# Optimization experiments

Measured on AMD Instinct MI355X. Metric: run time of the kernel, lower is better.

## Reference

```python
import jax, jax.numpy as jnp
import numpy as np

B, T = 32, 48
INPUT_DIM = 40000
TRAJ = 10
H = 256
OUT = 40000
TD = 48
L = 2
E = 128
DIN = E + TD  # 176


def setup_inputs() -> dict:
    key = jax.random.key(0)
    ks = jax.random.split(key, 16)
    s = 0.05
    inp = {
        "locations": jax.random.randint(ks[0], (B, T), 0, INPUT_DIM),
        "times": jax.random.randint(ks[1], (B, T), 0, TD),
        "labels": jax.random.randint(ks[2], (B,), 0, TRAJ),
        "embed_table": jax.random.normal(ks[3], (INPUT_DIM, E), dtype=jnp.float32) * s,
        "traj_table": jax.random.normal(ks[4], (TRAJ, H * L), dtype=jnp.float32) * s,
        "fc_w": jax.random.normal(ks[5], (OUT + TD, H), dtype=jnp.float32) * s,
        "fc_b": jnp.zeros((OUT + TD,), dtype=jnp.float32),
        "w_ih0": jax.random.normal(ks[6], (3 * H, DIN), dtype=jnp.float32) * s,
        "w_hh0": jax.random.normal(ks[7], (3 * H, H), dtype=jnp.float32) * s,
        "b_ih0": jnp.zeros((3 * H,), dtype=jnp.float32),
        "b_hh0": jnp.zeros((3 * H,), dtype=jnp.float32),
        "w_ih1": jax.random.normal(ks[8], (3 * H, H), dtype=jnp.float32) * s,
        "w_hh1": jax.random.normal(ks[9], (3 * H, H), dtype=jnp.float32) * s,
        "b_ih1": jnp.zeros((3 * H,), dtype=jnp.float32),
        "b_hh1": jnp.zeros((3 * H,), dtype=jnp.float32),
    }
    return inp


def gru_layer(x, h0, w_ih, w_hh, b_ih, b_hh):
    """PyTorch-semantics GRU layer. x: [T,B,din], h0: [B,H] -> [T,B,H]."""
    # precompute input projections for all timesteps (gates ordered r,z,n)
    xp = jnp.einsum('tbd,gd->tbg', x, w_ih) + b_ih  # [T,B,3H]

    def step(h, xp_t):
        hp = h @ w_hh.T + b_hh                      # [B,3H]
        xr, xz, xn = jnp.split(xp_t, 3, axis=-1)
        hr, hz, hn = jnp.split(hp, 3, axis=-1)
        r = jax.nn.sigmoid(xr + hr)
        z = jax.nn.sigmoid(xz + hz)
        n = jnp.tanh(xn + r * hn)
        h_new = (1.0 - z) * n + z * h
        return h_new, h_new

    _, ys = jax.lax.scan(step, h0, xp)
    return ys


def reference(locations, times, labels, embed_table, traj_table, fc_w, fc_b,
              w_ih0, w_hh0, b_ih0, b_hh0, w_ih1, w_hh1, b_ih1, b_hh1):
    x = embed_table[locations]                                  # [B,T,E]
    th = jax.nn.one_hot(times, TD, dtype=x.dtype)               # [B,T,TD]
    x = jnp.concatenate([x, th], axis=-1).transpose(1, 0, 2)    # [T,B,E+TD]
    # init_hidden: view (B, L*H) -> (L, -1, H), a raw reshape as in torch
    h0 = traj_table[labels].reshape(L, -1, H)                   # [L,B,H]
    y = gru_layer(x, h0[0], w_ih0, w_hh0, b_ih0, b_hh0)
    y = gru_layer(y, h0[1], w_ih1, w_hh1, b_ih1, b_hh1)         # [T,B,H]
    out = jax.nn.relu(y).transpose(1, 0, 2) @ fc_w.T + fc_b     # [B,T,OUT+TD]
    loc = jax.nn.log_softmax(out[..., :OUT], axis=-1)
    tm = jax.nn.log_softmax(out[..., OUT:], axis=-1)
    return loc, tm
```

## Files before the change

kernel.cpp:

```cpp
#include <hip/hip_runtime.h>
#include <math.h>

typedef __attribute__((ext_vector_type(4))) float f32x4;
typedef __attribute__((ext_vector_type(8))) short s16x8;

constexpr int B = 32, T = 48, H = 256, E = 128, TD = 48;
constexpr int OUT = 40000, NOUTC = 40048, NPADC = 40064;
constexpr int G3 = 768, DIN = 176;

__device__ __forceinline__ float sigmoidf_(float x){ return 1.f/(1.f+__expf(-x)); }
__device__ __forceinline__ float tanhf_(float x){
  float e = __expf(2.f*x);
  return 1.f - 2.f/(e + 1.f);
}
__device__ __forceinline__ unsigned short f2bf(float f){
  unsigned int u = __float_as_uint(f);
  u += 0x7fffu + ((u>>16)&1u);
  return (unsigned short)(u>>16);
}
__device__ __forceinline__ s16x8 pack8(float4 u, float4 v){
  s16x8 r;
  r[0]=(short)f2bf(u.x); r[1]=(short)f2bf(u.y); r[2]=(short)f2bf(u.z); r[3]=(short)f2bf(u.w);
  r[4]=(short)f2bf(v.x); r[5]=(short)f2bf(v.y); r[6]=(short)f2bf(v.z); r[7]=(short)f2bf(v.w);
  return r;
}
__device__ __forceinline__ void gl_lds16(const unsigned short* g, unsigned short* l){
  __builtin_amdgcn_global_load_lds((const __attribute__((address_space(1))) void*)g,
                                   (__attribute__((address_space(3))) void*)l, 16, 0, 0);
}
__device__ __forceinline__ void st_sc(unsigned* p, unsigned v){
  __hip_atomic_store(p, v, __ATOMIC_RELAXED, __HIP_MEMORY_SCOPE_SYSTEM);
}
__device__ __forceinline__ unsigned long long ld_sc64(const unsigned long long* p){
  return __hip_atomic_load(p, __ATOMIC_RELAXED, __HIP_MEMORY_SCOPE_SYSTEM);
}

__global__ void wt_kernel(const float* __restrict__ w_ih0, float* __restrict__ wT,
                          unsigned* __restrict__ bar){
  int i = blockIdx.x*256 + threadIdx.x;
  if (blockIdx.x == 0 && threadIdx.x == 0)
    __hip_atomic_store(bar, 0u, __ATOMIC_RELAXED, __HIP_MEMORY_SCOPE_SYSTEM);
  if (i >= E*G3) return;
  int e = i / G3, g = i % G3;
  wT[i] = w_ih0[g*DIN + e];
}

__global__ void xp0_kernel(const int* __restrict__ locations, const int* __restrict__ times,
                           const float* __restrict__ embed, const float* __restrict__ wT,
                           const float* __restrict__ w_ih0, const float* __restrict__ b_ih0,
                           float* __restrict__ xp0)
{
  __shared__ float emb_s[16][E];
  __shared__ int tm_s[16];
  const int r0 = blockIdx.x * 16;
  const int tid = threadIdx.x;
  for (int i = tid; i < 16*E; i += 256) {
    int p = i >> 7, e = i & 127;
    int r = r0 + p; int t = r >> 5, b = r & 31;
    emb_s[p][e] = embed[(size_t)locations[b*T + t]*E + e];
  }
  if (tid < 16) {
    int r = r0 + tid; int t = r >> 5, b = r & 31;
    tm_s[tid] = times[b*T + t];
  }
  __syncthreads();
  const int g = tid;
  float acc[16][3];
  #pragma unroll
  for (int p=0;p<16;p++){acc[p][0]=0.f;acc[p][1]=0.f;acc[p][2]=0.f;}
  for (int e = 0; e < E; e += 4) {
    float w0_[4], w1_[4], w2_[4];
    #pragma unroll
    for (int i=0;i<4;i++){
      w0_[i]=wT[(e+i)*G3 + g];
      w1_[i]=wT[(e+i)*G3 + 256 + g];
      w2_[i]=wT[(e+i)*G3 + 512 + g];
    }
    #pragma unroll
    for (int p=0;p<16;p++){
      float4 ev = *(const float4*)&emb_s[p][e];
      acc[p][0] += ev.x*w0_[0]+ev.y*w0_[1]+ev.z*w0_[2]+ev.w*w0_[3];
      acc[p][1] += ev.x*w1_[0]+ev.y*w1_[1]+ev.z*w1_[2]+ev.w*w1_[3];
      acc[p][2] += ev.x*w2_[0]+ev.y*w2_[1]+ev.z*w2_[2]+ev.w*w2_[3];
    }
  }
  #pragma unroll
  for (int p=0;p<16;p++){
    int r = r0+p; int tt = tm_s[p];
    xp0[(size_t)r*G3 + g]       = acc[p][0] + b_ih0[g]     + w_ih0[g*DIN       + E + tt];
    xp0[(size_t)r*G3 + 256 + g] = acc[p][1] + b_ih0[g+256] + w_ih0[(g+256)*DIN + E + tt];
    xp0[(size_t)r*G3 + 512 + g] = acc[p][2] + b_ih0[g+512] + w_ih0[(g+512)*DIN + E + tt];
  }
}

struct GruArgs {
  const float* xp0; const float* traj; const int* labels;
  const float* w_hh0; const float* b_hh0;
  const float* w_ih1; const float* w_hh1; const float* b_ih1; const float* b_hh1;
  unsigned short* exch;
  unsigned* bar;
  unsigned short* abf;
};

__global__ void __launch_bounds__(384, 2) gru_kernel(GruArgs a)
{
  __shared__ unsigned short Ash[2][32*264];
  __shared__ float gl0[3*32*17];
  __shared__ float gl1[4*32*17];
  __shared__ float hF0[512];
  __shared__ float hF1[512];
  const int tid  = threadIdx.x;
  const int jt   = blockIdx.x;
  const int wv   = tid >> 6;
  const int lane = tid & 63;
  const int g    = wv % 3, mt = wv / 3;
  const int fn   = lane & 15;
  const int fq   = lane >> 4;
  unsigned* exch32 = (unsigned*)a.exch;

  const int row = g*256 + jt*16 + fn;
  s16x8 b0[8], b1[16];
  #pragma unroll
  for (int kk = 0; kk < 8; ++kk) {
    const float* p0 = a.w_hh0 + (size_t)row*H + kk*32 + fq*8;
    const float* p1 = a.w_ih1 + (size_t)row*H + kk*32 + fq*8;
    const float* p2 = a.w_hh1 + (size_t)row*H + kk*32 + fq*8;
    b0[kk]    = pack8(*(const float4*)p0, *(const float4*)(p0+4));
    b1[kk]    = pack8(*(const float4*)p1, *(const float4*)(p1+4));
    b1[kk+8]  = pack8(*(const float4*)p2, *(const float4*)(p2+4));
  }

  for (int i = tid; i < 2*B*H; i += 384) {
    int l = i >> 13, bb = (i >> 8) & 31, h = i & 255;
    float v = a.traj[(size_t)a.labels[l*16 + (bb>>1)]*512 + (bb&1)*256 + h];
    Ash[l][bb*264 + h] = f2bf(v);
  }
  if (tid < 256) {
    int b = tid >> 3, jp = tid & 7, j0 = jp*2, gj = jt*16 + j0;
    float v00 = a.traj[(size_t)a.labels[(b>>1)]*512      + (b&1)*256 + gj];
    float v01 = a.traj[(size_t)a.labels[(b>>1)]*512      + (b&1)*256 + gj+1];
    float v10 = a.traj[(size_t)a.labels[16 + (b>>1)]*512 + (b&1)*256 + gj];
    float v11 = a.traj[(size_t)a.labels[16 + (b>>1)]*512 + (b&1)*256 + gj+1];
    hF0[b*16+j0] = v00; hF0[b*16+j0+1] = v01;
    hF1[b*16+j0] = v10; hF1[b*16+j0+1] = v11;
    st_sc(&exch32[(1*2+1)*4096 + b*128 + jt*8 + jp],
          (unsigned)f2bf(v10) | ((unsigned)f2bf(v11) << 16));
  }

  for (int p = 0; p <= T; ++p) {
    const int cur = p & 1, nxt = cur ^ 1;
    if (p) {
      const unsigned long long* src = (const unsigned long long*)a.exch + (size_t)cur*4096;
      unsigned long long v[11];
      #pragma unroll
      for (int k = 0; k < 11; ++k) {
        int i = tid + k*384;
        if (i < 4096) v[k] = ld_sc64(&src[i]);
      }
      #pragma unroll
      for (int k = 0; k < 11; ++k) {
        int i = tid + k*384;
        if (i < 4096) {
          int st = i >> 11, bb = (i >> 6) & 31, k4 = (i & 63) << 2;
          *(unsigned long long*)&Ash[st][bb*264 + k4] = v[k];
        }
      }
    }
    __syncthreads();

    if (p < T) {
      f32x4 acc = (f32x4){0.f,0.f,0.f,0.f};
      #pragma unroll
      for (int kk = 0; kk < 8; ++kk) {
        s16x8 af = *(const s16x8*)&Ash[0][(mt*16 + fn)*264 + kk*32 + fq*8];
        acc = __builtin_amdgcn_mfma_f32_16x16x32_bf16(af, b0[kk], acc, 0, 0, 0);
      }
      #pragma unroll
      for (int i = 0; i < 4; ++i)
        gl0[(g*32 + mt*16 + fq*4 + i)*17 + fn] = acc[i];
    }
    if (p >= 1) {
      if (g < 2) {
        f32x4 acc = (f32x4){0.f,0.f,0.f,0.f};
        #pragma unroll
        for (int kk = 0; kk < 8; ++kk) {
          s16x8 af = *(const s16x8*)&Ash[0][(mt*16 + fn)*264 + kk*32 + fq*8];
          acc = __builtin_amdgcn_mfma_f32_16x16x32_bf16(af, b1[kk], acc, 0, 0, 0);
        }
        #pragma unroll
        for (int kk = 0; kk < 8; ++kk) {
          s16x8 af = *(const s16x8*)&Ash[1][(mt*16 + fn)*264 + kk*32 + fq*8];
          acc = __builtin_amdgcn_mfma_f32_16x16x32_bf16(af, b1[8+kk], acc, 0, 0, 0);
        }
        #pragma unroll
        for (int i = 0; i < 4; ++i)
          gl1[(g*32 + mt*16 + fq*4 + i)*17 + fn] = acc[i];
      } else {
        f32x4 ax = (f32x4){0.f,0.f,0.f,0.f}, ah = (f32x4){0.f,0.f,0.f,0.f};
        #pragma unroll
        for (int kk = 0; kk < 8; ++kk) {
          s16x8 afx = *(const s16x8*)&Ash[0][(mt*16 + fn)*264 + kk*32 + fq*8];
          s16x8 afh = *(const s16x8*)&Ash[1][(mt*16 + fn)*264 + kk*32 + fq*8];
          ax = __builtin_amdgcn_mfma_f32_16x16x32_bf16(afx, b1[kk],   ax, 0, 0, 0);
          ah = __builtin_amdgcn_mfma_f32_16x16x32_bf16(afh, b1[8+kk], ah, 0, 0, 0);
        }
        #pragma unroll
        for (int i = 0; i < 4; ++i) {
          gl1[(2*32 + mt*16 + fq*4 + i)*17 + fn] = ax[i];
          gl1[(3*32 + mt*16 + fq*4 + i)*17 + fn] = ah[i];
        }
      }
    }
    __syncthreads();

    if (tid < 256) {
      const int b = tid >> 3, jp = tid & 7, j0 = jp*2, gj = jt*16 + j0;
      if (p < T) {
        const float* xp = a.xp0 + (size_t)(p*B + b)*G3 + gj;
        float r0 = sigmoidf_(xp[0]   + gl0[(b)*17+j0]      + a.b_hh0[gj]);
        float r1 = sigmoidf_(xp[1]   + gl0[(b)*17+j0+1]    + a.b_hh0[gj+1]);
        float z0 = sigmoidf_(xp[256] + gl0[(32+b)*17+j0]   + a.b_hh0[256+gj]);
        float z1 = sigmoidf_(xp[257] + gl0[(32+b)*17+j0+1] + a.b_hh0[256+gj+1]);
        float n0 = tanhf_(xp[512] + r0*(gl0[(64+b)*17+j0]   + a.b_hh0[512+gj]));
        float n1 = tanhf_(xp[513] + r1*(gl0[(64+b)*17+j0+1] + a.b_hh0[512+gj+1]));
        float h0n = (1.f - z0)*n0 + z0*hF0[b*16+j0];
        float h1n = (1.f - z1)*n1 + z1*hF0[b*16+j0+1];
        hF0[b*16+j0] = h0n; hF0[b*16+j0+1] = h1n;
        st_sc(&exch32[(nxt*2 + 0)*4096 + b*128 + jt*8 + jp],
              (unsigned)f2bf(h0n) | ((unsigned)f2bf(h1n) << 16));
      }
      if (p >= 1) {
        const int t1 = p - 1;
        float r0 = sigmoidf_(gl1[(b)*17+j0]      + a.b_ih1[gj]     + a.b_hh1[gj]);
        float r1 = sigmoidf_(gl1[(b)*17+j0+1]    + a.b_ih1[gj+1]   + a.b_hh1[gj+1]);
        float z0 = sigmoidf_(gl1[(32+b)*17+j0]   + a.b_ih1[256+gj]   + a.b_hh1[256+gj]);
        float z1 = sigmoidf_(gl1[(32+b)*17+j0+1] + a.b_ih1[256+gj+1] + a.b_hh1[256+gj+1]);
        float n0 = tanhf_(gl1[(64+b)*17+j0]   + a.b_ih1[512+gj]
                          + r0*(gl1[(96+b)*17+j0]   + a.b_hh1[512+gj]));
        float n1 = tanhf_(gl1[(64+b)*17+j0+1] + a.b_ih1[512+gj+1]
                          + r1*(gl1[(96+b)*17+j0+1] + a.b_hh1[512+gj+1]));
        float h0n = (1.f - z0)*n0 + z0*hF1[b*16+j0];
        float h1n = (1.f - z1)*n1 + z1*hF1[b*16+j0+1];
        hF1[b*16+j0] = h0n; hF1[b*16+j0+1] = h1n;
        st_sc(&exch32[(nxt*2 + 1)*4096 + b*128 + jt*8 + jp],
              (unsigned)f2bf(h0n) | ((unsigned)f2bf(h1n) << 16));
        ((unsigned*)a.abf)[((size_t)(b*T + t1)*H + gj) >> 1] =
              (unsigned)f2bf(fmaxf(h0n,0.f)) | ((unsigned)f2bf(fmaxf(h1n,0.f)) << 16);
      }
    }
    if (p == T) break;

    asm volatile("s_waitcnt vmcnt(0)" ::: "memory");
    __syncthreads();
    if (tid == 0) {
      __hip_atomic_fetch_add(a.bar, 1u, __ATOMIC_RELAXED, __HIP_MEMORY_SCOPE_SYSTEM);
      const unsigned tgt = 16u*(unsigned)(p + 1);
      unsigned it = 0;
      while (__hip_atomic_load(a.bar, __ATOMIC_RELAXED, __HIP_MEMORY_SCOPE_SYSTEM) < tgt) {
        if (++it > (1u<<21)) break;
      }
    }
    __syncthreads();
  }
}

__global__ void castw_kernel(const float* __restrict__ fcw, unsigned short* __restrict__ wbf){
  int g = blockIdx.x*256 + threadIdx.x;
  if (g >= NPADC*64) return;
  int row = g >> 6;
  ushort4 o;
  if (row < NOUTC) {
    float4 v = ((const float4*)fcw)[g];
    o.x=f2bf(v.x); o.y=f2bf(v.y); o.z=f2bf(v.z); o.w=f2bf(v.w);
  } else { o.x=0; o.y=0; o.z=0; o.w=0; }
  ((ushort4*)wbf)[g] = o;
}

__global__ void __launch_bounds__(256) gemm_kernel(const unsigned short* __restrict__ Abf,
                                                   const unsigned short* __restrict__ Wbf,
                                                   const float* __restrict__ fc_b,
                                                   float* __restrict__ dout)
{
  __shared__ unsigned short As[128*32];
  __shared__ unsigned short Ws[128*32];
  const int m0 = blockIdx.x * 128;
  const int n0 = blockIdx.y * 128;
  const int tid = threadIdx.x;
  const int lane = tid & 63;
  const int wv = tid >> 6;
  f32x4 acc[2][8];
  #pragma unroll
  for (int i=0;i<2;i++)
    #pragma unroll
    for(int jx=0;jx<8;jx++) acc[i][jx] = (f32x4){0.f,0.f,0.f,0.f};

  const int srow = tid >> 2;
  const int skoff = (tid & 3) * 8;
  const unsigned short* aptr = Abf + (size_t)(m0 + srow)*256 + skoff;
  const unsigned short* wptr = Wbf + (size_t)(n0 + srow)*256 + skoff;
  unsigned short* asd = &As[tid*8];
  unsigned short* wsd = &Ws[tid*8];

  const int fr = lane & 15;
  const int fk = (lane >> 4) * 8;

  for (int kk = 0; kk < 256; kk += 32) {
    gl_lds16(aptr + kk,            asd);
    gl_lds16(aptr + 64*256 + kk,   asd + 64*32);
    gl_lds16(wptr + kk,            wsd);
    gl_lds16(wptr + 64*256 + kk,   wsd + 64*32);
    __syncthreads();
    s16x8 a0 = *(const s16x8*)&As[(wv*32 + fr)*32 + fk];
    s16x8 a1 = *(const s16x8*)&As[(wv*32 + 16 + fr)*32 + fk];
    #pragma unroll
    for (int ct = 0; ct < 8; ++ct) {
      s16x8 bfr = *(const s16x8*)&Ws[(ct*16 + fr)*32 + fk];
      acc[0][ct] = __builtin_amdgcn_mfma_f32_16x16x32_bf16(a0, bfr, acc[0][ct], 0, 0, 0);
      acc[1][ct] = __builtin_amdgcn_mfma_f32_16x16x32_bf16(a1, bfr, acc[1][ct], 0, 0, 0);
    }
    __syncthreads();
  }

  const int quad = lane >> 4;
  #pragma unroll
  for (int rt = 0; rt < 2; ++rt) {
    #pragma unroll
    for (int ct = 0; ct < 8; ++ct) {
      int col = n0 + ct*16 + fr;
      if (col < NOUTC) {
        float bias = fc_b[col];
        #pragma unroll
        for (int i = 0; i < 4; ++i) {
          int row = m0 + wv*32 + rt*16 + quad*4 + i;
          float v = acc[rt][ct][i] + bias;
          if (col < OUT) dout[(size_t)row*OUT + col] = v;
          else dout[(size_t)OUT*B*T + (size_t)row*TD + (col - OUT)] = v;
        }
      }
    }
  }
}

__global__ void stats_kernel(const float* __restrict__ dout, float* __restrict__ logz){
  const int r = blockIdx.x;
  const float4* row = (const float4*)(dout + (size_t)r*OUT);
  float m = -INFINITY, s = 0.f;
  for (int i = threadIdx.x; i < OUT/4; i += 256) {
    float4 v = row[i];
    float mx = fmaxf(fmaxf(v.x,v.y), fmaxf(v.z,v.w));
    if (mx > m) { s *= __expf(m - mx); m = mx; }
    s += __expf(v.x-m)+__expf(v.y-m)+__expf(v.z-m)+__expf(v.w-m);
  }
  #pragma unroll
  for (int off = 1; off < 64; off <<= 1) {
    float m2 = __shfl_xor(m, off);
    float s2 = __shfl_xor(s, off);
    float nm = fmaxf(m, m2);
    s = s*__expf(m-nm) + s2*__expf(m2-nm);
    m = nm;
  }
  __shared__ float sm[4], ss[4];
  if ((threadIdx.x & 63) == 0){ sm[threadIdx.x>>6]=m; ss[threadIdx.x>>6]=s; }
  __syncthreads();
  if (threadIdx.x == 0){
    float M=sm[0], S=ss[0];
    #pragma unroll
    for (int w=1;w<4;w++){
      float nm=fmaxf(M,sm[w]); S = S*__expf(M-nm)+ss[w]*__expf(sm[w]-nm); M=nm;
    }
    logz[r] = M + logf(S);
  }
}

__global__ void norm_kernel(float* __restrict__ dout, const float* __restrict__ logz){
  size_t i = (size_t)blockIdx.x*256 + threadIdx.x;
  if (i >= (size_t)B*T*OUT/4) return;
  int r = (int)(i / (OUT/4));
  float lz = logz[r];
  float4* p = (float4*)dout + i;
  float4 v = *p;
  v.x -= lz; v.y -= lz; v.z -= lz; v.w -= lz;
  *p = v;
}

__global__ void tm_kernel(float* __restrict__ dout){
  const int r = blockIdx.x;
  const int lane = threadIdx.x;
  float* base = dout + (size_t)OUT*B*T + (size_t)r*TD;
  float v = (lane < TD) ? base[lane] : -INFINITY;
  float m = v;
  #pragma unroll
  for (int off=32; off; off>>=1) m = fmaxf(m, __shfl_xor(m, off));
  float e = (lane < TD) ? __expf(v - m) : 0.f;
  float s = e;
  #pragma unroll
  for (int off=32; off; off>>=1) s += __shfl_xor(s, off);
  float lz = m + logf(s);
  if (lane < TD) base[lane] = v - lz;
}

extern "C" void kernel_launch(void* const* d_in, const int* in_sizes, int n_in,
                              void* d_out, int out_size, void* d_ws, size_t ws_size,
                              hipStream_t stream)
{
  const int*   locations = (const int*)d_in[0];
  const int*   times     = (const int*)d_in[1];
  const int*   labels    = (const int*)d_in[2];
  const float* embed     = (const float*)d_in[3];
  const float* traj      = (const float*)d_in[4];
  const float* fc_w      = (const float*)d_in[5];
  const float* fc_b      = (const float*)d_in[6];
  const float* w_ih0     = (const float*)d_in[7];
  const float* w_hh0     = (const float*)d_in[8];
  const float* b_ih0     = (const float*)d_in[9];
  const float* b_hh0     = (const float*)d_in[10];
  const float* w_ih1     = (const float*)d_in[11];
  const float* w_hh1     = (const float*)d_in[12];
  const float* b_ih1     = (const float*)d_in[13];
  const float* b_hh1     = (const float*)d_in[14];
  float* out = (float*)d_out;
  char* ws = (char*)d_ws;

  float* xp0            = (float*)(ws);
  unsigned short* exch  = (unsigned short*)(ws + 4718592);
  unsigned* bar         = (unsigned*)(ws + 4784128);
  float* logz           = (float*)(ws + 4784384);
  unsigned short* abf   = (unsigned short*)(ws + 4790528);
  unsigned short* wbf   = (unsigned short*)(ws + 5576960);
  float* wT             = (float*)(ws + 26089728);

  castw_kernel<<<dim3((NPADC*64 + 255)/256), dim3(256), 0, stream>>>(fc_w, wbf);
  wt_kernel<<<dim3((E*G3 + 255)/256), dim3(256), 0, stream>>>(w_ih0, wT, bar);
  xp0_kernel<<<dim3(96), dim3(256), 0, stream>>>(locations, times, embed, wT, w_ih0, b_ih0, xp0);

  GruArgs ga{xp0, traj, labels, w_hh0, b_hh0, w_ih1, w_hh1, b_ih1, b_hh1,
             exch, bar, abf};
  void* kargs[] = { &ga };
  hipLaunchCooperativeKernel((void*)gru_kernel, dim3(16), dim3(384), kargs, 0, stream);

  gemm_kernel<<<dim3(12, 313), dim3(256), 0, stream>>>(abf, wbf, fc_b, out);
  stats_kernel<<<dim3(B*T), dim3(256), 0, stream>>>(out, logz);
  norm_kernel<<<dim3((B*T*OUT/4 + 255)/256), dim3(256), 0, stream>>>(out, logz);
  tm_kernel<<<dim3(B*T), dim3(64), 0, stream>>>(out);
}
```

Baseline: 772.0 us.

## Replace grid barrier with step-tagged exchange slots for GRU hidden-state handoff

Removes the per-timestep global atomic counter barrier in the cooperative GRU kernel. Each hidden-state exchange word now carries its timestep tag in the upper 32 bits, and readers spin on their own slots until the expected tag appears. This avoids the fetch-add, the single-thread spin and two block-wide syncs per step. In exchange it doubles the exchange payload to 64-bit words and adds per-thread polling loops with more registers (launch bounds lowered to one block per CU).

Result: slower. 827.9 us (+7.2%).

```diff
diff --git a/kernel.cpp b/kernel.cpp
--- a/kernel.cpp
+++ b/kernel.cpp
@@ -28,18 +28,17 @@
   __builtin_amdgcn_global_load_lds((const __attribute__((address_space(1))) void*)g,
                                    (__attribute__((address_space(3))) void*)l, 16, 0, 0);
 }
-__device__ __forceinline__ void st_sc(unsigned* p, unsigned v){
+__device__ __forceinline__ void st_sc64(unsigned long long* p, unsigned long long v){
   __hip_atomic_store(p, v, __ATOMIC_RELAXED, __HIP_MEMORY_SCOPE_SYSTEM);
 }
 __device__ __forceinline__ unsigned long long ld_sc64(const unsigned long long* p){
-  return __hip_atomic_load(p, __ATOMIC_RELAXED, __HIP_MEMORY_SCOPE_SYSTEM);
+  return __hip_atomic_load((unsigned long long*)p, __ATOMIC_RELAXED, __HIP_MEMORY_SCOPE_SYSTEM);
 }
 
 __global__ void wt_kernel(const float* __restrict__ w_ih0, float* __restrict__ wT,
-                          unsigned* __restrict__ bar){
+                          unsigned long long* __restrict__ exch64){
   int i = blockIdx.x*256 + threadIdx.x;
-  if (blockIdx.x == 0 && threadIdx.x == 0)
-    __hip_atomic_store(bar, 0u, __ATOMIC_RELAXED, __HIP_MEMORY_SCOPE_SYSTEM);
+  if (i < 16384) st_sc64(&exch64[i], 0ull);
   if (i >= E*G3) return;
   int e = i / G3, g = i % G3;
   wT[i] = w_ih0[g*DIN + e];
@@ -97,12 +96,11 @@
   const float* xp0; const float* traj; const int* labels;
   const float* w_hh0; const float* b_hh0;
   const float* w_ih1; const float* w_hh1; const float* b_ih1; const float* b_hh1;
-  unsigned short* exch;
-  unsigned* bar;
+  unsigned long long* exch;
   unsigned short* abf;
 };
 
-__global__ void __launch_bounds__(384, 2) gru_kernel(GruArgs a)
+__global__ void __launch_bounds__(384, 1) gru_kernel(GruArgs a)
 {
   __shared__ unsigned short Ash[2][32*264];
   __shared__ float gl0[3*32*17];
@@ -116,7 +114,6 @@
   const int g    = wv % 3, mt = wv / 3;
   const int fn   = lane & 15;
   const int fq   = lane >> 4;
-  unsigned* exch32 = (unsigned*)a.exch;
 
   const int row = g*256 + jt*16 + fn;
   s16x8 b0[8], b1[16];
@@ -143,26 +140,43 @@
     float v11 = a.traj[(size_t)a.labels[16 + (b>>1)]*512 + (b&1)*256 + gj+1];
     hF0[b*16+j0] = v00; hF0[b*16+j0+1] = v01;
     hF1[b*16+j0] = v10; hF1[b*16+j0+1] = v11;
-    st_sc(&exch32[(1*2+1)*4096 + b*128 + jt*8 + jp],
-          (unsigned)f2bf(v10) | ((unsigned)f2bf(v11) << 16));
+    unsigned pay = (unsigned)f2bf(v10) | ((unsigned)f2bf(v11) << 16);
+    st_sc64(&a.exch[(size_t)(1*2 + 1)*4096 + b*128 + jt*8 + jp],
+            (unsigned long long)pay | (1ull << 32));
   }
 
   for (int p = 0; p <= T; ++p) {
     const int cur = p & 1, nxt = cur ^ 1;
     if (p) {
-      const unsigned long long* src = (const unsigned long long*)a.exch + (size_t)cur*4096;
-      unsigned long long v[11];
+      const unsigned long long* src = a.exch + (size_t)cur*8192;
+      const unsigned want = (unsigned)p;
+      unsigned long long v[22];
       #pragma unroll
-      for (int k = 0; k < 11; ++k) {
+      for (int k = 0; k < 22; ++k) {
         int i = tid + k*384;
-        if (i < 4096) v[k] = ld_sc64(&src[i]);
-      }
+        if (i < 8192) v[k] = ld_sc64(&src[i]);
+      }
+      unsigned pend = 0;
       #pragma unroll
-      for (int k = 0; k < 11; ++k) {
+      for (int k = 0; k < 22; ++k) {
         int i = tid + k*384;
-        if (i < 4096) {
-          int st = i >> 11, bb = (i >> 6) & 31, k4 = (i & 63) << 2;
-          *(unsigned long long*)&Ash[st][bb*264 + k4] = v[k];
+        if (i < 8192 && (unsigned)(v[k] >> 32) != want) pend |= (1u << k);
+      }
+      int guard = 0;
+      while (pend && ++guard < (1 << 20)) {
+        #pragma unroll
+        for (int k = 0; k < 22; ++k)
+          if (pend & (1u << k)) v[k] = ld_sc64(&src[tid + k*384]);
+        #pragma unroll
+        for (int k = 0; k < 22; ++k)
+          if ((pend & (1u << k)) && (unsigned)(v[k] >> 32) == want) pend &= ~(1u << k);
+      }
+      #pragma unroll
+      for (int k = 0; k < 22; ++k) {
+        int i = tid + k*384;
+        if (i < 8192) {
+          int st = i >> 12, bb = (i >> 7) & 31, cp = i & 127;
+          *(unsigned*)&Ash[st][bb*264 + cp*2] = (unsigned)v[k];
         }
       }
     }
@@ -215,6 +229,7 @@
 
     if (tid < 256) {
       const int b = tid >> 3, jp = tid & 7, j0 = jp*2, gj = jt*16 + j0;
+      const unsigned long long tagw = ((unsigned long long)(unsigned)(p + 1)) << 32;
       if (p < T) {
         const float* xp = a.xp0 + (size_t)(p*B + b)*G3 + gj;
         float r0 = sigmoidf_(xp[0]   + gl0[(b)*17+j0]      + a.b_hh0[gj]);
@@ -226,8 +241,9 @@
         float h0n = (1.f - z0)*n0 + z0*hF0[b*16+j0];
         float h1n = (1.f - z1)*n1 + z1*hF0[b*16+j0+1];
         hF0[b*16+j0] = h0n; hF0[b*16+j0+1] = h1n;
-        st_sc(&exch32[(nxt*2 + 0)*4096 + b*128 + jt*8 + jp],
-              (unsigned)f2bf(h0n) | ((unsigned)f2bf(h1n) << 16));
+        unsigned pay = (unsigned)f2bf(h0n) | ((unsigned)f2bf(h1n) << 16);
+        st_sc64(&a.exch[(size_t)(nxt*2 + 0)*4096 + b*128 + jt*8 + jp],
+                (unsigned long long)pay | tagw);
       }
       if (p >= 1) {
         const int t1 = p - 1;
@@ -242,25 +258,13 @@
         float h0n = (1.f - z0)*n0 + z0*hF1[b*16+j0];
         float h1n = (1.f - z1)*n1 + z1*hF1[b*16+j0+1];
         hF1[b*16+j0] = h0n; hF1[b*16+j0+1] = h1n;
-        st_sc(&exch32[(nxt*2 + 1)*4096 + b*128 + jt*8 + jp],
-              (unsigned)f2bf(h0n) | ((unsigned)f2bf(h1n) << 16));
+        unsigned pay = (unsigned)f2bf(h0n) | ((unsigned)f2bf(h1n) << 16);
+        st_sc64(&a.exch[(size_t)(nxt*2 + 1)*4096 + b*128 + jt*8 + jp],
+                (unsigned long long)pay | tagw);
         ((unsigned*)a.abf)[((size_t)(b*T + t1)*H + gj) >> 1] =
               (unsigned)f2bf(fmaxf(h0n,0.f)) | ((unsigned)f2bf(fmaxf(h1n,0.f)) << 16);
       }
     }
-    if (p == T) break;
-
-    asm volatile("s_waitcnt vmcnt(0)" ::: "memory");
-    __syncthreads();
-    if (tid == 0) {
-      __hip_atomic_fetch_add(a.bar, 1u, __ATOMIC_RELAXED, __HIP_MEMORY_SCOPE_SYSTEM);
-      const unsigned tgt = 16u*(unsigned)(p + 1);
-      unsigned it = 0;
-      while (__hip_atomic_load(a.bar, __ATOMIC_RELAXED, __HIP_MEMORY_SCOPE_SYSTEM) < tgt) {
-        if (++it > (1u<<21)) break;
-      }
-    }
-    __syncthreads();
   }
 }
 
@@ -421,20 +425,19 @@
   float* out = (float*)d_out;
   char* ws = (char*)d_ws;
 
-  float* xp0            = (float*)(ws);
-  unsigned short* exch  = (unsigned short*)(ws + 4718592);
-  unsigned* bar         = (unsigned*)(ws + 4784128);
-  float* logz           = (float*)(ws + 4784384);
-  unsigned short* abf   = (unsigned short*)(ws + 4790528);
-  unsigned short* wbf   = (unsigned short*)(ws + 5576960);
-  float* wT             = (float*)(ws + 26089728);
+  float* xp0                 = (float*)(ws);
+  unsigned long long* exch   = (unsigned long long*)(ws + 4718592);
+  float* logz                = (float*)(ws + 4849664);
+  unsigned short* abf        = (unsigned short*)(ws + 4855808);
+  unsigned short* wbf        = (unsigned short*)(ws + 5642240);
+  float* wT                  = (float*)(ws + 26155008);
 
   castw_kernel<<<dim3((NPADC*64 + 255)/256), dim3(256), 0, stream>>>(fc_w, wbf);
-  wt_kernel<<<dim3((E*G3 + 255)/256), dim3(256), 0, stream>>>(w_ih0, wT, bar);
+  wt_kernel<<<dim3((E*G3 + 255)/256), dim3(256), 0, stream>>>(w_ih0, wT, exch);
   xp0_kernel<<<dim3(96), dim3(256), 0, stream>>>(locations, times, embed, wT, w_ih0, b_ih0, xp0);
 
   GruArgs ga{xp0, traj, labels, w_hh0, b_hh0, w_ih1, w_hh1, b_ih1, b_hh1,
-             exch, bar, abf};
+             exch, abf};
   void* kargs[] = { &ga };
   hipLaunchCooperativeKernel((void*)gru_kernel, dim3(16), dim3(384), kargs, 0, stream);
 
```
